# Performance work log

Hardware: AMD Instinct MI355X
Metric: run time of the kernel (lower is better)

## Reference

```python
import jax, jax.numpy as jnp
import numpy as np
from jax import lax

EPS = 1e-06
B, C, T = 64, 80, 8000

def _inverse_sigmoid(v):
    v = min(1.0 - 1e-4, max(1e-4, float(v)))
    return float(np.log(v / (1.0 - v)))

def setup_inputs() -> dict:
    key = jax.random.key(0)
    features = jax.random.normal(key, (B, C, T), dtype=jnp.float32)
    logit_s = jnp.full((C,), _inverse_sigmoid(0.04), dtype=jnp.float32)
    alpha = jnp.full((C,), 0.96, dtype=jnp.float32)
    delta = jnp.full((C,), 2.0, dtype=jnp.float32)
    log_r = jnp.full((C,), np.log(0.5), dtype=jnp.float32)
    return {"features": features, "logit_s": logit_s, "alpha": alpha,
            "delta": delta, "log_r": log_r}

def reference(features, logit_s, alpha, delta, log_r):
    # features: [B, C, T]
    x = jnp.maximum(features, 0.0)
    s = jax.nn.sigmoid(logit_s)                      # [C]
    a = jnp.clip(alpha, 0.1, 1.0)[None, :, None]     # [1,C,1]
    d = jnp.maximum(delta, 0.1)[None, :, None]
    r = jnp.clip(jnp.exp(log_r), 0.05, 1.5)[None, :, None]
    # first-order IIR smoother m_t = (1-s)*m_{t-1} + s*x_t, m_0 = x_0
    xt = jnp.moveaxis(x, -1, 0)                      # [T, B, C]
    def step(prev, x_cur):
        cur = (1.0 - s) * prev + s * x_cur
        return cur, cur
    _, ms = lax.scan(step, xt[0], xt[1:])            # [T-1, B, C]
    m = jnp.concatenate([xt[:1], ms], axis=0)        # [T, B, C]
    m = jnp.moveaxis(m, 0, -1)                       # [B, C, T]
    pcen = jnp.power(x / jnp.power(EPS + m, a) + d, r) - jnp.power(d, r)
    return pcen
```

## Files before the change

### kernel.cpp

```cpp
#include <hip/hip_runtime.h>
#include <math.h>

#define PCEN_EPS 1e-6f

constexpr int Bn = 64, Cn = 80, Tn = 8000;
constexpr int ROWS = Bn * Cn;
constexpr int WPR  = 4;
constexpr int SEG  = Tn / WPR;
constexpr int EPL  = 8;
constexpr int LCH  = 64 * EPL;
constexpr int NCH  = (SEG + LCH - 1) / LCH;

__device__ __forceinline__ float fast_pow_pos(float b, float e) {
#if __has_builtin(__builtin_amdgcn_logf) && __has_builtin(__builtin_amdgcn_exp2f)
    return __builtin_amdgcn_exp2f(e * __builtin_amdgcn_logf(b));
#else
    return __exp2f(e * __log2f(b));
#endif
}

__global__ __launch_bounds__(256, 4)
void pcen_kernel(const float* __restrict__ x,
                 const float* __restrict__ logit_s,
                 const float* __restrict__ alpha,
                 const float* __restrict__ delta,
                 const float* __restrict__ log_r,
                 float* __restrict__ out)
{
    __shared__ float sm[WPR];
    const int lane = threadIdx.x & 63;
    const int wid  = threadIdx.x >> 6;
    const int row  = blockIdx.x;
    const int c    = row % Cn;

    const float s  = 1.0f / (1.0f + __expf(-logit_s[c]));
    const float w  = 1.0f - s;
    const float a  = fminf(fmaxf(alpha[c], 0.1f), 1.0f);
    const float dd = fmaxf(delta[c], 0.1f);
    const float rr = fminf(fmaxf(__expf(log_r[c]), 0.05f), 1.5f);
    const float d_r = fast_pow_pos(dd, rr);
    const float na  = -a;

    float w8p[8];
    {
        const float w2 = w * w, w4 = w2 * w2;
        w8p[0] = w4 * w4;
        #pragma unroll
        for (int i = 1; i < 8; ++i) w8p[i] = w8p[i - 1] * w8p[i - 1];
    }
    float w8L = 1.0f;
    #pragma unroll
    for (int b = 0; b < 6; ++b)
        if (lane & (1 << b)) w8L *= w8p[b];
    const float w512 = w8p[6];
    const float w2000 = w8p[7] * w8p[6] * w8p[5] * w8p[4] * w8p[3] * w8p[1];

    const float* __restrict__ xs = x   + (size_t)row * Tn + wid * SEG;
    float* __restrict__ os       = out + (size_t)row * Tn + wid * SEG;

    float xv[NCH][EPL];
    #pragma unroll
    for (int ch = 0; ch < NCH; ++ch) {
        const int base = ch * LCH + lane * EPL;
        if (base + EPL <= SEG) {
            const float4 p0 = *reinterpret_cast<const float4*>(xs + base);
            const float4 p1 = *reinterpret_cast<const float4*>(xs + base + 4);
            xv[ch][0] = p0.x; xv[ch][1] = p0.y; xv[ch][2] = p0.z; xv[ch][3] = p0.w;
            xv[ch][4] = p1.x; xv[ch][5] = p1.y; xv[ch][6] = p1.z; xv[ch][7] = p1.w;
        } else {
            #pragma unroll
            for (int j = 0; j < EPL; ++j) xv[ch][j] = 0.0f;
        }
    }
    #pragma unroll
    for (int ch = 0; ch < NCH; ++ch)
        #pragma unroll
        for (int j = 0; j < EPL; ++j) xv[ch][j] = fmaxf(xv[ch][j], 0.0f);

    float P = __shfl(xv[0][0], 0, 64);
    if (wid != 0) P = 0.0f;

    float mv[NCH][EPL];
    #pragma unroll
    for (int ch = 0; ch < NCH; ++ch) {
        float y = s * xv[ch][0];
        #pragma unroll
        for (int j = 1; j < EPL; ++j) y = fmaf(y, w, s * xv[ch][j]);
        float Y = y;
        #pragma unroll
        for (int st = 0; st < 6; ++st) {
            const float Yup  = __shfl_up(Y, 1 << st, 64);
            const float cand = fmaf(w8p[st], Yup, Y);
            Y = (lane >= (1 << st)) ? cand : Y;
        }
        const float Yprev = __shfl_up(Y, 1, 64);
        const float excl  = (lane == 0) ? 0.0f : Yprev;
        const float F     = fmaf(w8L, P, excl);
        float mm = F;
        #pragma unroll
        for (int j = 0; j < EPL; ++j) { mm = fmaf(w, mm, s * xv[ch][j]); mv[ch][j] = mm; }
        P = __shfl(mv[ch][EPL - 1], (ch == NCH - 1) ? 57 : 63, 64);
    }

    if (lane == 0) sm[wid] = P;
    __syncthreads();
    const float A0 = sm[0];
    const float A1 = fmaf(w2000, A0, sm[1]);
    const float A2 = fmaf(w2000, A1, sm[2]);
    const float Pin = (wid == 1) ? A0 : (wid == 2) ? A1 : (wid == 3) ? A2 : 0.0f;

    float wc = 1.0f;
    #pragma unroll
    for (int ch = 0; ch < NCH; ++ch) {
        float f = wc * w8L * w;
        float ov[EPL];
        #pragma unroll
        for (int j = 0; j < EPL; ++j) {
            const float m = fmaf(f, Pin, mv[ch][j]);
            f *= w;
            const float t = fast_pow_pos(PCEN_EPS + m, na);
            ov[j] = fast_pow_pos(fmaf(xv[ch][j], t, dd), rr) - d_r;
        }
        const int base = ch * LCH + lane * EPL;
        if (base + EPL <= SEG) {
            *reinterpret_cast<float4*>(os + base)     = make_float4(ov[0], ov[1], ov[2], ov[3]);
            *reinterpret_cast<float4*>(os + base + 4) = make_float4(ov[4], ov[5], ov[6], ov[7]);
        }
        wc *= w512;
    }
}

extern "C" void kernel_launch(void* const* d_in, const int* in_sizes, int n_in,
                              void* d_out, int out_size, void* d_ws, size_t ws_size,
                              hipStream_t stream) {
    const float* features = (const float*)d_in[0];
    const float* logit_s  = (const float*)d_in[1];
    const float* alpha    = (const float*)d_in[2];
    const float* delta    = (const float*)d_in[3];
    const float* log_r    = (const float*)d_in[4];
    float* out = (float*)d_out;

    pcen_kernel<<<ROWS, WPR * 64, 0, stream>>>(features, logit_s, alpha, delta, log_r, out);
}
```

Baseline: 63.88 us.

## Use 16 elements per lane and defer smoother recomputation to cut registers

Each lane now holds 16 elements per chunk, so the 2000-element segment needs 2 chunks instead of 4. The per-element smoothed values are no longer stored. Each chunk's carry is derived from the scanned prefix, and the recursion is replayed in the emit pass with the cross-wave carry folded into the starting value. This lowers register pressure and allows a launch bound of 8 blocks per SM, at the cost of computing the serial recursion twice and running longer dependent chains per lane.

```diff
diff --git a/kernel.cpp b/kernel.cpp
--- a/kernel.cpp
+++ b/kernel.cpp
@@ -7,9 +7,9 @@
 constexpr int ROWS = Bn * Cn;
 constexpr int WPR  = 4;
 constexpr int SEG  = Tn / WPR;
-constexpr int EPL  = 8;
+constexpr int EPL  = 16;
 constexpr int LCH  = 64 * EPL;
-constexpr int NCH  = (SEG + LCH - 1) / LCH;
+constexpr int NCH  = 2;
 
 __device__ __forceinline__ float fast_pow_pos(float b, float e) {
 #if __has_builtin(__builtin_amdgcn_logf) && __has_builtin(__builtin_amdgcn_exp2f)
@@ -19,7 +19,7 @@
 #endif
 }
 
-__global__ __launch_bounds__(256, 4)
+__global__ __launch_bounds__(256, 8)
 void pcen_kernel(const float* __restrict__ x,
                  const float* __restrict__ logit_s,
                  const float* __restrict__ alpha,
@@ -41,19 +41,20 @@
     const float d_r = fast_pow_pos(dd, rr);
     const float na  = -a;
 
-    float w8p[8];
+    float w16p[7];
     {
-        const float w2 = w * w, w4 = w2 * w2;
-        w8p[0] = w4 * w4;
+        const float w2 = w * w, w4 = w2 * w2, w8 = w4 * w4;
+        w16p[0] = w8 * w8;
         #pragma unroll
-        for (int i = 1; i < 8; ++i) w8p[i] = w8p[i - 1] * w8p[i - 1];
+        for (int i = 1; i < 7; ++i) w16p[i] = w16p[i - 1] * w16p[i - 1];
     }
-    float w8L = 1.0f;
+    float w16L = 1.0f;
     #pragma unroll
     for (int b = 0; b < 6; ++b)
-        if (lane & (1 << b)) w8L *= w8p[b];
-    const float w512 = w8p[6];
-    const float w2000 = w8p[7] * w8p[6] * w8p[5] * w8p[4] * w8p[3] * w8p[1];
+        if (lane & (1 << b)) w16L *= w16p[b];
+    const float w1024 = w16p[6];
+    const float w976  = w16p[5] * w16p[4] * w16p[3] * w16p[2] * w16p[0];
+    const float w2000 = w1024 * w976;
 
     const float* __restrict__ xs = x   + (size_t)row * Tn + wid * SEG;
     float* __restrict__ os       = out + (size_t)row * Tn + wid * SEG;
@@ -63,10 +64,12 @@
     for (int ch = 0; ch < NCH; ++ch) {
         const int base = ch * LCH + lane * EPL;
         if (base + EPL <= SEG) {
-            const float4 p0 = *reinterpret_cast<const float4*>(xs + base);
-            const float4 p1 = *reinterpret_cast<const float4*>(xs + base + 4);
-            xv[ch][0] = p0.x; xv[ch][1] = p0.y; xv[ch][2] = p0.z; xv[ch][3] = p0.w;
-            xv[ch][4] = p1.x; xv[ch][5] = p1.y; xv[ch][6] = p1.z; xv[ch][7] = p1.w;
+            #pragma unroll
+            for (int q = 0; q < 4; ++q) {
+                const float4 p = *reinterpret_cast<const float4*>(xs + base + 4 * q);
+                xv[ch][4 * q + 0] = p.x; xv[ch][4 * q + 1] = p.y;
+                xv[ch][4 * q + 2] = p.z; xv[ch][4 * q + 3] = p.w;
+            }
         } else {
             #pragma unroll
             for (int j = 0; j < EPL; ++j) xv[ch][j] = 0.0f;
@@ -77,30 +80,30 @@
         #pragma unroll
         for (int j = 0; j < EPL; ++j) xv[ch][j] = fmaxf(xv[ch][j], 0.0f);
 
-    float P = __shfl(xv[0][0], 0, 64);
-    if (wid != 0) P = 0.0f;
+    const float p00 = __shfl(xv[0][0], 0, 64);
+    float P = (wid == 0) ? p00 : 0.0f;
 
-    float mv[NCH][EPL];
-    #pragma unroll
-    for (int ch = 0; ch < NCH; ++ch) {
-        float y = s * xv[ch][0];
+    float F0, F1;
+    auto scanChunk = [&](const float (&xc)[EPL], float Pprev, float wP,
+                         int lastLane, float& Fout) -> float {
+        float y = s * xc[0];
         #pragma unroll
-        for (int j = 1; j < EPL; ++j) y = fmaf(y, w, s * xv[ch][j]);
+        for (int j = 1; j < EPL; ++j) y = fmaf(y, w, s * xc[j]);
         float Y = y;
         #pragma unroll
         for (int st = 0; st < 6; ++st) {
             const float Yup  = __shfl_up(Y, 1 << st, 64);
-            const float cand = fmaf(w8p[st], Yup, Y);
+            const float cand = fmaf(w16p[st], Yup, Y);
             Y = (lane >= (1 << st)) ? cand : Y;
         }
         const float Yprev = __shfl_up(Y, 1, 64);
         const float excl  = (lane == 0) ? 0.0f : Yprev;
-        const float F     = fmaf(w8L, P, excl);
-        float mm = F;
-        #pragma unroll
-        for (int j = 0; j < EPL; ++j) { mm = fmaf(w, mm, s * xv[ch][j]); mv[ch][j] = mm; }
-        P = __shfl(mv[ch][EPL - 1], (ch == NCH - 1) ? 57 : 63, 64);
-    }
+        Fout = fmaf(w16L, Pprev, excl);
+        const float Ylast = __shfl(Y, lastLane, 64);
+        return fmaf(wP, Pprev, Ylast);
+    };
+    P = scanChunk(xv[0], P, w1024, 63, F0);
+    P = scanChunk(xv[1], P, w976, 60, F1);
 
     if (lane == 0) sm[wid] = P;
     __syncthreads();
@@ -109,25 +112,26 @@
     const float A2 = fmaf(w2000, A1, sm[2]);
     const float Pin = (wid == 1) ? A0 : (wid == 2) ? A1 : (wid == 3) ? A2 : 0.0f;
 
-    float wc = 1.0f;
-    #pragma unroll
-    for (int ch = 0; ch < NCH; ++ch) {
-        float f = wc * w8L * w;
-        float ov[EPL];
-        #pragma unroll
-        for (int j = 0; j < EPL; ++j) {
-            const float m = fmaf(f, Pin, mv[ch][j]);
-            f *= w;
-            const float t = fast_pow_pos(PCEN_EPS + m, na);
-            ov[j] = fast_pow_pos(fmaf(xv[ch][j], t, dd), rr) - d_r;
+    auto emit = [&](const float (&xc)[EPL], float Fc, int base) {
+        if (base + EPL <= SEG) {
+            float mm = Fc;
+            #pragma unroll
+            for (int q = 0; q < 4; ++q) {
+                float o[4];
+                #pragma unroll
+                for (int j = 0; j < 4; ++j) {
+                    const float xx = xc[4 * q + j];
+                    mm = fmaf(w, mm, s * xx);
+                    const float t = fast_pow_pos(PCEN_EPS + mm, na);
+                    o[j] = fast_pow_pos(fmaf(xx, t, dd), rr) - d_r;
+                }
+                *reinterpret_cast<float4*>(os + base + 4 * q) =
+                    make_float4(o[0], o[1], o[2], o[3]);
+            }
         }
-        const int base = ch * LCH + lane * EPL;
-        if (base + EPL <= SEG) {
-            *reinterpret_cast<float4*>(os + base)     = make_float4(ov[0], ov[1], ov[2], ov[3]);
-            *reinterpret_cast<float4*>(os + base + 4) = make_float4(ov[4], ov[5], ov[6], ov[7]);
-        }
-        wc *= w512;
-    }
+    };
+    emit(xv[0], fmaf(w16L, Pin, F0), lane * EPL);
+    emit(xv[1], fmaf(w1024 * w16L, Pin, F1), LCH + lane * EPL);
 }
 
 extern "C" void kernel_launch(void* const* d_in, const int* in_sizes, int n_in,
```

Result: slower. 149.2 us (+133.6%).
